# Kernel tuning notes

Measured on AMD Instinct MI355X. Metric: run time of the kernel, lower is better.

Reference implementation:

```python
import jax, jax.numpy as jnp
import numpy as np

N, E, F_IN, DIM, HEADS = 16384, 262144, 128, 64, 4
HID = DIM * HEADS  # 256
NEG = 0.2


def _lin(k, fan_in, fan_out):
    kw, kb = jax.random.split(k)
    s = 1.0 / np.sqrt(fan_in)
    return (jax.random.uniform(kw, (fan_in, fan_out), jnp.float32, -s, s),
            jax.random.uniform(kb, (fan_out,), jnp.float32, -s, s))


def setup_inputs() -> dict:
    key = jax.random.key(0)
    ks = jax.random.split(key, 20)
    x = jax.random.normal(ks[0], (N, F_IN), jnp.float32)
    edge_index = jax.random.randint(ks[1], (2, E), 0, N, jnp.int32)
    Win, b_in = _lin(ks[2], F_IN, DIM)
    Wskip, bskip = _lin(ks[3], DIM, HID)
    # conv1: in=DIM, out per head=DIM, heads=HEADS, concat -> HID
    Wl1, _ = _lin(ks[4], DIM, HID)
    Wr1, _ = _lin(ks[5], DIM, HID)
    att1 = jax.random.normal(ks[6], (HEADS, DIM), jnp.float32) * 0.1
    b1 = jnp.zeros((HID,), jnp.float32)
    # conv2: in=HID, out=HID, heads=1, concat=False
    Wl2, _ = _lin(ks[7], HID, HID)
    Wr2, _ = _lin(ks[8], HID, HID)
    att2 = jax.random.normal(ks[9], (1, HID), jnp.float32) * 0.1
    b2 = jnp.zeros((HID,), jnp.float32)
    # conv3: in=HID, out=HID, heads=1, concat=False
    Wl3, _ = _lin(ks[10], HID, HID)
    Wr3, _ = _lin(ks[11], HID, HID)
    att3 = jax.random.normal(ks[12], (1, HID), jnp.float32) * 0.1
    b3 = jnp.zeros((HID,), jnp.float32)
    Wm1, bm1 = _lin(ks[13], HID, DIM)
    Wm2, bm2 = _lin(ks[14], DIM, DIM)
    Wm3, bm3 = _lin(ks[15], DIM, 1)
    return dict(x=x, edge_index=edge_index, Win=Win, b_in=b_in,
                Wskip=Wskip, bskip=bskip,
                Wl1=Wl1, Wr1=Wr1, att1=att1, b1=b1,
                Wl2=Wl2, Wr2=Wr2, att2=att2, b2=b2,
                Wl3=Wl3, Wr3=Wr3, att3=att3, b3=b3,
                Wm1=Wm1, bm1=bm1, Wm2=Wm2, bm2=bm2, Wm3=Wm3, bm3=bm3)


def gatv2(x, src, dst, Wl, Wr, att, b, concat):
    # PyG GATv2Conv: x_l = lin_l(x)[src], x_r = lin_r(x)[dst]
    n = x.shape[0]
    H, D = att.shape
    xl = (x @ Wl).reshape(n, H, D)
    xr = (x @ Wr).reshape(n, H, D)
    e = jax.nn.leaky_relu(xl[src] + xr[dst], NEG)          # [E, H, D]
    logits = jnp.einsum('ehd,hd->eh', e, att)              # [E, H]
    m = jax.ops.segment_max(logits, dst, num_segments=n)   # per-dst softmax
    alpha = jnp.exp(logits - m[dst])
    denom = jax.ops.segment_sum(alpha, dst, num_segments=n)
    alpha = alpha / denom[dst]
    out = jax.ops.segment_sum(alpha[:, :, None] * xl[src], dst, num_segments=n)
    out = out.reshape(n, H * D) if concat else out.mean(axis=1)
    return out + b


def reference(x, edge_index, Win, b_in, Wskip, bskip,
              Wl1, Wr1, att1, b1, Wl2, Wr2, att2, b2,
              Wl3, Wr3, att3, b3, Wm1, bm1, Wm2, bm2, Wm3, bm3):
    n = x.shape[0]
    # add self loops (GATv2Conv default add_self_loops=True)
    loop = jnp.arange(n, dtype=edge_index.dtype)
    src = jnp.concatenate([edge_index[0], loop])
    dst = jnp.concatenate([edge_index[1], loop])

    h = jax.nn.relu(x @ Win + b_in)                         # [N, DIM]
    out1 = jax.nn.relu(gatv2(h, src, dst, Wl1, Wr1, att1, b1, True))
    out1 = out1 + (h @ Wskip + bskip)                       # [N, HID]
    out2 = jax.nn.relu(gatv2(out1, src, dst, Wl2, Wr2, att2, b2, False))
    out2 = out2 + out1
    out3 = jax.nn.relu(gatv2(out2, src, dst, Wl3, Wr3, att3, b3, False))
    out3 = out3 + out2
    out = jax.nn.relu(out3 @ Wm1 + bm1)
    out = jax.nn.relu(out @ Wm2 + bm2)
    out = out @ Wm3 + bm3                                   # [N, 1]
    return out.reshape(-1)
```

## Files before the change

kernel.cpp:

```cpp
#include <hip/hip_runtime.h>
#include <cstdint>
#include <cstddef>

#define N_NODES 16384
#define E_EDGES 262144
#define FIN     128
#define DIM     64
#define HID     256
#define NEG     0.2f

typedef _Float16 h8 __attribute__((ext_vector_type(8)));
typedef _Float16 h4 __attribute__((ext_vector_type(4)));
typedef _Float16 h2 __attribute__((ext_vector_type(2)));
typedef float    f32x4 __attribute__((ext_vector_type(4)));
typedef float    f32x2 __attribute__((ext_vector_type(2)));

__global__ __launch_bounds__(256) void hist_kernel(const int* __restrict__ dst,
                                                   int* __restrict__ cnt) {
    int i = blockIdx.x * 256 + threadIdx.x;
    if (i < E_EDGES) atomicAdd(&cnt[dst[i]], 1);
}

__global__ __launch_bounds__(256) void csr_scan_kernel(const int* __restrict__ cnt,
                                                       int* __restrict__ offs,
                                                       int* __restrict__ cursor) {
    __shared__ int wsum[4];
    int tid = threadIdx.x, lane = tid & 63, w = tid >> 6;
    int base = tid * 64;
    const int4* c4 = (const int4*)(cnt + base);
    int4 v[16];
    int s = 0;
#pragma unroll
    for (int i = 0; i < 16; ++i) {
        v[i] = c4[i];
        s += v[i].x + v[i].y + v[i].z + v[i].w;
    }
    int scan = s;
#pragma unroll
    for (int off = 1; off < 64; off <<= 1) {
        int t = __shfl_up(scan, off);
        if (lane >= off) scan += t;
    }
    if (lane == 63) wsum[w] = scan;
    __syncthreads();
    int wbase = 0;
#pragma unroll
    for (int i = 0; i < 4; ++i) if (i < w) wbase += wsum[i];
    int run = wbase + (scan - s);
#pragma unroll
    for (int i = 0; i < 16; ++i) {
        int4 o;
        o.x = run;
        o.y = o.x + v[i].x;
        o.z = o.y + v[i].y;
        o.w = o.z + v[i].z;
        *(int4*)(offs + base + 4 * i) = o;
        *(int4*)(cursor + base + 4 * i) = o;
        run = o.w + v[i].w;
    }
    if (tid == 255) offs[N_NODES] = run;
}

__global__ __launch_bounds__(256) void scatter_kernel(const int* __restrict__ src,
                                                      const int* __restrict__ dst,
                                                      int* __restrict__ cursor,
                                                      int* __restrict__ esrc) {
    int i = blockIdx.x * 256 + threadIdx.x;
    if (i < E_EDGES) {
        int p = atomicAdd(&cursor[dst[i]], 1);
        esrc[p] = src[i];
    }
}

struct PackJob { const float* W; _Float16* dst; int Ksrc, Nsrc, NT, colOff; };
struct PackJobs { PackJob j[10]; };

__global__ __launch_bounds__(256) void pack_all_kernel(PackJobs jobs, int* __restrict__ cnt) {
    int i = blockIdx.x * 256 + threadIdx.x;
    if (blockIdx.y == 10) {
        if (i < N_NODES) cnt[i] = 0;
        return;
    }
    PackJob jb = jobs.j[blockIdx.y];
    if (i < jb.Ksrc * jb.Nsrc) {
        int k = i / jb.Nsrc, n = i % jb.Nsrc;
        jb.dst[((size_t)(k >> 3) * jb.NT + jb.colOff + n) * 8 + (k & 7)] = (_Float16)jb.W[i];
    }
}

template<int K, bool RELU, bool O16, bool IN32>
__global__ __launch_bounds__(64) void mfma_n64_kernel(const void* __restrict__ Av,
                                                      const _Float16* __restrict__ Wp,
                                                      const float* __restrict__ bias,
                                                      void* __restrict__ outv) {
    int lane = threadIdx.x;
    int rowBase = blockIdx.x * 64;
    int l15 = lane & 15, l4 = lane >> 4;

    f32x4 acc[4][4] = {};
#pragma unroll
    for (int ks = 0; ks < K / 32; ++ks) {
        h8 af[4], bf[4];
#pragma unroll
        for (int mi = 0; mi < 4; ++mi) {
            if constexpr (IN32) {
                const float* ap = (const float*)Av + (size_t)(rowBase + mi * 16 + l15) * K + ks * 32 + l4 * 8;
                float4 a0 = *(const float4*)ap;
                float4 a1 = *(const float4*)(ap + 4);
                h8 v;
                v[0] = (_Float16)a0.x; v[1] = (_Float16)a0.y;
                v[2] = (_Float16)a0.z; v[3] = (_Float16)a0.w;
                v[4] = (_Float16)a1.x; v[5] = (_Float16)a1.y;
                v[6] = (_Float16)a1.z; v[7] = (_Float16)a1.w;
                af[mi] = v;
            } else {
                af[mi] = *(const h8*)((const _Float16*)Av + (size_t)(rowBase + mi * 16 + l15) * K + ks * 32 + l4 * 8);
            }
        }
#pragma unroll
        for (int ni = 0; ni < 4; ++ni)
            bf[ni] = *(const h8*)(Wp + ((size_t)(ks * 4 + l4) * 64 + ni * 16 + l15) * 8);
#pragma unroll
        for (int mi = 0; mi < 4; ++mi)
#pragma unroll
            for (int ni = 0; ni < 4; ++ni)
                acc[mi][ni] = __builtin_amdgcn_mfma_f32_16x16x32_f16(af[mi], bf[ni], acc[mi][ni], 0, 0, 0);
    }
#pragma unroll
    for (int mi = 0; mi < 4; ++mi)
#pragma unroll
        for (int ni = 0; ni < 4; ++ni) {
            int c = ni * 16 + l15;
            float bv = bias[c];
#pragma unroll
            for (int q = 0; q < 4; ++q) {
                int r = rowBase + mi * 16 + l4 * 4 + q;
                float v = acc[mi][ni][q] + bv;
                if (RELU) v = fmaxf(v, 0.f);
                if constexpr (O16) ((_Float16*)outv)[(size_t)r * 64 + c] = (_Float16)v;
                else               ((float*)outv)[(size_t)r * 64 + c] = v;
            }
        }
}

template<int K>
__global__ __launch_bounds__(256) void mfma_gemm_kernel(const _Float16* __restrict__ A,
                                                        const _Float16* __restrict__ Wp,
                                                        int NT,
                                                        _Float16* __restrict__ o16a,
                                                        _Float16* __restrict__ o16b,
                                                        float* __restrict__ o32,
                                                        const float* __restrict__ bias) {
    int tid = threadIdx.x;
    int lane = tid & 63, wid = tid >> 6;
    int wm = wid >> 1, wn = wid & 1;
    int rowBase = blockIdx.x * 128 + wm * 64;
    int colBase = blockIdx.y * 128 + wn * 64;
    int l15 = lane & 15, l4 = lane >> 4;

    f32x4 acc[4][4] = {};
#pragma unroll
    for (int ks = 0; ks < K / 32; ++ks) {
        h8 af[4], bf[4];
#pragma unroll
        for (int mi = 0; mi < 4; ++mi)
            af[mi] = *(const h8*)(A + (size_t)(rowBase + mi * 16 + l15) * K + ks * 32 + l4 * 8);
#pragma unroll
        for (int ni = 0; ni < 4; ++ni)
            bf[ni] = *(const h8*)(Wp + ((size_t)(ks * 4 + l4) * NT + colBase + ni * 16 + l15) * 8);
#pragma unroll
        for (int mi = 0; mi < 4; ++mi)
#pragma unroll
            for (int ni = 0; ni < 4; ++ni)
                acc[mi][ni] = __builtin_amdgcn_mfma_f32_16x16x32_f16(af[mi], bf[ni], acc[mi][ni], 0, 0, 0);
    }

    int seg = colBase >> 8;
    int cbase = colBase & 255;
    if (o32 != nullptr && seg == 2) {
#pragma unroll
        for (int mi = 0; mi < 4; ++mi)
#pragma unroll
            for (int ni = 0; ni < 4; ++ni) {
                int c = cbase + ni * 16 + l15;
                float bv = bias[c];
#pragma unroll
                for (int q = 0; q < 4; ++q) {
                    int r = rowBase + mi * 16 + l4 * 4 + q;
                    o32[(size_t)r * 256 + c] = acc[mi][ni][q] + bv;
                }
            }
    } else {
        _Float16* o = (seg == 0) ? o16a : o16b;
#pragma unroll
        for (int mi = 0; mi < 4; ++mi)
#pragma unroll
            for (int ni = 0; ni < 4; ++ni) {
                int c = cbase + ni * 16 + l15;
#pragma unroll
                for (int q = 0; q < 4; ++q) {
                    int r = rowBase + mi * 16 + l4 * 4 + q;
                    o[(size_t)r * 256 + c] = (_Float16)acc[mi][ni][q];
                }
            }
    }
}

template<int H, int OMODE>
__global__ __launch_bounds__(256) void gat_agg_kernel(const _Float16* __restrict__ xl,
                                                      const _Float16* __restrict__ xr,
                                                      const float* __restrict__ att,
                                                      const float* __restrict__ bias,
                                                      const float* __restrict__ resid,
                                                      const int* __restrict__ offs,
                                                      const int* __restrict__ esrc,
                                                      float* __restrict__ out,
                                                      _Float16* __restrict__ out16) {
    int tid = threadIdx.x;
    int wid = tid >> 6;
    int lane = tid & 63;
    int node = blockIdx.x * 4 + wid;
    int g  = lane >> 4;
    int li = lane & 15;

    h2 xrv[8];
    {
        const h8* xp = (const h8*)(xr + ((size_t)node << 8) + (li << 4));
        h8 a0 = xp[0], a1 = xp[1];
#pragma unroll
        for (int i = 0; i < 4; ++i) { xrv[i][0] = a0[2 * i]; xrv[i][1] = a0[2 * i + 1]; }
#pragma unroll
        for (int i = 0; i < 4; ++i) { xrv[4 + i][0] = a1[2 * i]; xrv[4 + i][1] = a1[2 * i + 1]; }
    }
    h2 attv[8];
    {
        const float4* ap = (const float4*)(att + (li << 4));
#pragma unroll
        for (int i = 0; i < 4; ++i) {
            float4 a = ap[i];
            attv[2 * i][0] = (_Float16)a.x; attv[2 * i][1] = (_Float16)a.y;
            attv[2 * i + 1][0] = (_Float16)a.z; attv[2 * i + 1][1] = (_Float16)a.w;
        }
    }
    const h2 negc = { (_Float16)NEG, (_Float16)NEG };

    int dbase = (li << 4) + (g << 2);
    float4 bv = *(const float4*)(bias + dbase);
    float4 rv = *(const float4*)(resid + ((size_t)node << 8) + dbase);

    float m = -1e30f, s = 0.f;
    f32x2 acc2[8];
#pragma unroll
    for (int i = 0; i < 8; ++i) acc2[i] = (f32x2){0.f, 0.f};

    int e0 = offs[node];
    int total = offs[node + 1] - e0 + 1;

    auto gather = [&](int srcn, h2* hv) {
        const h8* xp = (const h8*)(xl + ((size_t)srcn << 8) + (li << 4));
        h8 a0 = xp[0], a1 = xp[1];
#pragma unroll
        for (int i = 0; i < 4; ++i) { hv[i][0] = a0[2 * i]; hv[i][1] = a0[2 * i + 1]; }
#pragma unroll
        for (int i = 0; i < 4; ++i) { hv[4 + i][0] = a1[2 * i]; hv[4 + i][1] = a1[2 * i + 1]; }
    };
    auto logit = [&](const h2* hv) -> float {
        float p0 = 0.f, p1 = 0.f;
#pragma unroll
        for (int i = 0; i < 4; ++i) {
            h2 sum = hv[i] + xrv[i];
            h2 lr = __builtin_elementwise_max(sum, sum * negc);
            p0 = __builtin_amdgcn_fdot2(lr, attv[i], p0, false);
            h2 sum2 = hv[4 + i] + xrv[4 + i];
            h2 lr2 = __builtin_elementwise_max(sum2, sum2 * negc);
            p1 = __builtin_amdgcn_fdot2(lr2, attv[4 + i], p1, false);
        }
        float part = p0 + p1;
        part += __shfl_xor(part, 1);
        part += __shfl_xor(part, 2);
        if constexpr (H == 1) {
            part += __shfl_xor(part, 4);
            part += __shfl_xor(part, 8);
        }
        return part;
    };

    int vi = g;
    int sA = 0, sB = 0;
    if (vi + 4 < total) {
        sA = (vi == 0) ? node : esrc[e0 + vi - 1];
        sB = esrc[e0 + vi + 3];
    }
    for (; vi + 4 < total; vi += 8) {
        int nvi = vi + 8;
        int ia = e0 + nvi - 1; if (ia > E_EDGES - 1) ia = E_EDGES - 1;
        int ib = e0 + nvi + 3; if (ib > E_EDGES - 1) ib = E_EDGES - 1;
        int sA2 = esrc[ia];
        int sB2 = esrc[ib];

        h2 hA[8], hB[8];
        gather(sA, hA);
        gather(sB, hB);
        float lpA = logit(hA);
        float lpB = logit(hB);
        float mx = fmaxf(lpA, lpB);
        if (mx > m + 8.f) {
            float c  = __expf(m - mx);
            float pA = __expf(lpA - mx);
            float pB = __expf(lpB - mx);
            s = s * c + pA + pB;
#pragma unroll
            for (int i = 0; i < 8; ++i) {
                f32x2 t = acc2[i] * c;
                t[0] = fmaf(pA, (float)hA[i][0], t[0]);
                t[1] = fmaf(pA, (float)hA[i][1], t[1]);
                t[0] = fmaf(pB, (float)hB[i][0], t[0]);
                t[1] = fmaf(pB, (float)hB[i][1], t[1]);
                acc2[i] = t;
            }
            m = mx;
        } else {
            float pA = __expf(lpA - m);
            float pB = __expf(lpB - m);
            s += pA + pB;
#pragma unroll
            for (int i = 0; i < 8; ++i) {
                f32x2 t = acc2[i];
                t[0] = fmaf(pA, (float)hA[i][0], t[0]);
                t[1] = fmaf(pA, (float)hA[i][1], t[1]);
                t[0] = fmaf(pB, (float)hB[i][0], t[0]);
                t[1] = fmaf(pB, (float)hB[i][1], t[1]);
                acc2[i] = t;
            }
        }
        sA = sA2; sB = sB2;
    }
    for (; vi < total; vi += 4) {
        int srcn = (vi == 0) ? node : esrc[e0 + vi - 1];
        h2 hA[8];
        gather(srcn, hA);
        float lp = logit(hA);
        if (lp > m + 8.f) {
            float c = __expf(m - lp);
            float p = 1.f;
            s = s * c + p;
#pragma unroll
            for (int i = 0; i < 8; ++i) {
                f32x2 t = acc2[i] * c;
                t[0] = fmaf(p, (float)hA[i][0], t[0]);
                t[1] = fmaf(p, (float)hA[i][1], t[1]);
                acc2[i] = t;
            }
            m = lp;
        } else {
            float p = __expf(lp - m);
            s += p;
#pragma unroll
            for (int i = 0; i < 8; ++i) {
                f32x2 t = acc2[i];
                t[0] = fmaf(p, (float)hA[i][0], t[0]);
                t[1] = fmaf(p, (float)hA[i][1], t[1]);
                acc2[i] = t;
            }
        }
    }

#pragma unroll
    for (int mask = 16; mask <= 32; mask <<= 1) {
        float m2 = __shfl_xor(m, mask);
        float s2 = __shfl_xor(s, mask);
        float M = fmaxf(m, m2);
        float c1 = __expf(m - M);
        float c2 = __expf(m2 - M);
        s = s * c1 + s2 * c2;
#pragma unroll
        for (int i = 0; i < 8; ++i) {
            float ax = __shfl_xor(acc2[i][0], mask);
            float ay = __shfl_xor(acc2[i][1], mask);
            acc2[i][0] = acc2[i][0] * c1 + ax * c2;
            acc2[i][1] = acc2[i][1] * c1 + ay * c2;
        }
        m = M;
    }

    float inv = 1.f / s;
    float a0, a1v, a2, a3;
    if (g == 0)      { a0 = acc2[0][0]; a1v = acc2[0][1]; a2 = acc2[1][0]; a3 = acc2[1][1]; }
    else if (g == 1) { a0 = acc2[2][0]; a1v = acc2[2][1]; a2 = acc2[3][0]; a3 = acc2[3][1]; }
    else if (g == 2) { a0 = acc2[4][0]; a1v = acc2[4][1]; a2 = acc2[5][0]; a3 = acc2[5][1]; }
    else             { a0 = acc2[6][0]; a1v = acc2[6][1]; a2 = acc2[7][0]; a3 = acc2[7][1]; }
    float o0 = fmaxf(a0 * inv + bv.x, 0.f) + rv.x;
    float o1 = fmaxf(a1v * inv + bv.y, 0.f) + rv.y;
    float o2 = fmaxf(a2 * inv + bv.z, 0.f) + rv.z;
    float o3 = fmaxf(a3 * inv + bv.w, 0.f) + rv.w;
    if constexpr (OMODE != 2) {
        float4 ov = make_float4(o0, o1, o2, o3);
        *(float4*)(out + ((size_t)node << 8) + dbase) = ov;
    }
    if constexpr (OMODE != 0) {
        h4 hv;
        hv[0] = (_Float16)o0; hv[1] = (_Float16)o1;
        hv[2] = (_Float16)o2; hv[3] = (_Float16)o3;
        *(h4*)(out16 + ((size_t)node << 8) + dbase) = hv;
    }
}

__global__ __launch_bounds__(256) void mlp_head_kernel(const _Float16* __restrict__ A,
                                                       const _Float16* __restrict__ Wm1p,
                                                       const float* __restrict__ bm1,
                                                       const _Float16* __restrict__ Wm2p,
                                                       const float* __restrict__ bm2,
                                                       const float* __restrict__ Wm3,
                                                       const float* __restrict__ bm3,
                                                       float* __restrict__ out) {
    __shared__ _Float16 t1s[4][16][72];
    int tid = threadIdx.x;
    int lane = tid & 63, wid = tid >> 6;
    int rowBase = blockIdx.x * 64 + wid * 16;
    int l15 = lane & 15, l4 = lane >> 4;

    f32x4 acc[4] = {};
#pragma unroll
    for (int ks = 0; ks < 8; ++ks) {
        h8 af = *(const h8*)(A + (size_t)(rowBase + l15) * 256 + ks * 32 + l4 * 8);
        h8 bf[4];
#pragma unroll
        for (int ni = 0; ni < 4; ++ni)
            bf[ni] = *(const h8*)(Wm1p + ((size_t)(ks * 4 + l4) * 64 + ni * 16 + l15) * 8);
#pragma unroll
        for (int ni = 0; ni < 4; ++ni)
            acc[ni] = __builtin_amdgcn_mfma_f32_16x16x32_f16(af, bf[ni], acc[ni], 0, 0, 0);
    }
#pragma unroll
    for (int ni = 0; ni < 4; ++ni) {
        int c = ni * 16 + l15;
        float bv = bm1[c];
#pragma unroll
        for (int q = 0; q < 4; ++q)
            t1s[wid][l4 * 4 + q][c] = (_Float16)fmaxf(acc[ni][q] + bv, 0.f);
    }

    f32x4 acc2[4] = {};
#pragma unroll
    for (int ks = 0; ks < 2; ++ks) {
        h8 af = *(const h8*)&t1s[wid][l15][ks * 32 + l4 * 8];
        h8 bf[4];
#pragma unroll
        for (int ni = 0; ni < 4; ++ni)
            bf[ni] = *(const h8*)(Wm2p + ((size_t)(ks * 4 + l4) * 64 + ni * 16 + l15) * 8);
#pragma unroll
        for (int ni = 0; ni < 4; ++ni)
            acc2[ni] = __builtin_amdgcn_mfma_f32_16x16x32_f16(af, bf[ni], acc2[ni], 0, 0, 0);
    }

    float b3 = bm3[0];
    float b2v[4], w3v[4];
#pragma unroll
    for (int ni = 0; ni < 4; ++ni) {
        b2v[ni] = bm2[ni * 16 + l15];
        w3v[ni] = Wm3[ni * 16 + l15];
    }
#pragma unroll
    for (int q = 0; q < 4; ++q) {
        float part = 0.f;
#pragma unroll
        for (int ni = 0; ni < 4; ++ni)
            part += fmaxf(acc2[ni][q] + b2v[ni], 0.f) * w3v[ni];
        part += __shfl_xor(part, 1);
        part += __shfl_xor(part, 2);
        part += __shfl_xor(part, 4);
        part += __shfl_xor(part, 8);
        if (l15 == 0)
            out[rowBase + l4 * 4 + q] = part + b3;
    }
}

extern "C" void kernel_launch(void* const* d_in, const int* in_sizes, int n_in,
                              void* d_out, int out_size, void* d_ws, size_t ws_size,
                              hipStream_t stream) {
    const float* x     = (const float*)d_in[0];
    const int*   ei    = (const int*)d_in[1];
    const float* Win   = (const float*)d_in[2];
    const float* b_in  = (const float*)d_in[3];
    const float* Wskip = (const float*)d_in[4];
    const float* bskip = (const float*)d_in[5];
    const float* Wl1   = (const float*)d_in[6];
    const float* Wr1   = (const float*)d_in[7];
    const float* att1  = (const float*)d_in[8];
    const float* b1    = (const float*)d_in[9];
    const float* Wl2   = (const float*)d_in[10];
    const float* Wr2   = (const float*)d_in[11];
    const float* att2  = (const float*)d_in[12];
    const float* b2    = (const float*)d_in[13];
    const float* Wl3   = (const float*)d_in[14];
    const float* Wr3   = (const float*)d_in[15];
    const float* att3  = (const float*)d_in[16];
    const float* b3    = (const float*)d_in[17];
    const float* Wm1   = (const float*)d_in[18];
    const float* bm1   = (const float*)d_in[19];
    const float* Wm2   = (const float*)d_in[20];
    const float* bm2   = (const float*)d_in[21];
    const float* Wm3   = (const float*)d_in[22];
    const float* bm3   = (const float*)d_in[23];

    char* p = (char*)d_ws;
    auto alloc = [&](size_t bytes) { char* r = p; p += (bytes + 255) & ~(size_t)255; return r; };
    const size_t NN = N_NODES;
    float*    skip = (float*)alloc(NN * 256 * 4);
    float*    out1 = (float*)alloc(NN * 256 * 4);
    _Float16* o116 = (_Float16*)alloc(NN * 256 * 2);
    _Float16* o216 = (_Float16*)alloc(NN * 256 * 2);
    _Float16* o316 = o116;
    _Float16* h16  = (_Float16*)alloc(NN * 64 * 2);
    _Float16* xl16 = (_Float16*)alloc(NN * 256 * 2);
    _Float16* xr16 = (_Float16*)alloc(NN * 256 * 2);
    _Float16* Wp1  = (_Float16*)alloc((size_t)64 * 768 * 2);
    _Float16* Wp2  = (_Float16*)alloc((size_t)256 * 512 * 2);
    _Float16* Wp3  = (_Float16*)alloc((size_t)256 * 512 * 2);
    _Float16* Winp = (_Float16*)alloc((size_t)128 * 64 * 2);
    _Float16* Wm1p = (_Float16*)alloc((size_t)256 * 64 * 2);
    _Float16* Wm2p = (_Float16*)alloc((size_t)64 * 64 * 2);
    int* cnt    = (int*)alloc(N_NODES * 4);
    int* offs   = (int*)alloc((N_NODES + 1) * 4);
    int* cursor = (int*)alloc(N_NODES * 4);
    int* esrc   = (int*)alloc(E_EDGES * 4);

    const int* src = ei;
    const int* dst = ei + E_EDGES;

    PackJobs jobs = {{
        { Wl1,   Wp1,  64,  256, 768, 0   },
        { Wr1,   Wp1,  64,  256, 768, 256 },
        { Wskip, Wp1,  64,  256, 768, 512 },
        { Wl2,   Wp2,  256, 256, 512, 0   },
        { Wr2,   Wp2,  256, 256, 512, 256 },
        { Wl3,   Wp3,  256, 256, 512, 0   },
        { Wr3,   Wp3,  256, 256, 512, 256 },
        { Win,   Winp, 128, 64,  64,  0   },
        { Wm1,   Wm1p, 256, 64,  64,  0   },
        { Wm2,   Wm2p, 64,  64,  64,  0   },
    }};
    pack_all_kernel<<<dim3(256, 11), 256, 0, stream>>>(jobs, cnt);

    hist_kernel<<<E_EDGES / 256, 256, 0, stream>>>(dst, cnt);
    csr_scan_kernel<<<1, 256, 0, stream>>>(cnt, offs, cursor);
    scatter_kernel<<<E_EDGES / 256, 256, 0, stream>>>(src, dst, cursor, esrc);

    mfma_n64_kernel<128, true, true, true><<<N_NODES / 64, 64, 0, stream>>>(x, Winp, b_in, h16);

    mfma_gemm_kernel<64><<<dim3(128, 6), 256, 0, stream>>>(h16, Wp1, 768, xl16, xr16, skip, bskip);
    gat_agg_kernel<4, 1><<<N_NODES / 4, 256, 0, stream>>>(xl16, xr16, att1, b1, skip, offs, esrc, out1, o116);

    mfma_gemm_kernel<256><<<dim3(128, 4), 256, 0, stream>>>(o116, Wp2, 512, xl16, xr16, nullptr, nullptr);
    gat_agg_kernel<1, 1><<<N_NODES / 4, 256, 0, stream>>>(xl16, xr16, att2, b2, out1, offs, esrc, skip , o216);

    mfma_gemm_kernel<256><<<dim3(128, 4), 256, 0, stream>>>(o216, Wp3, 512, xl16, xr16, nullptr, nullptr);
    gat_agg_kernel<1, 2><<<N_NODES / 4, 256, 0, stream>>>(xl16, xr16, att3, b3, skip , offs, esrc, nullptr, o316);

    mlp_head_kernel<<<N_NODES / 64, 256, 0, stream>>>(o316, Wm1p, bm1, Wm2p, bm2, Wm3, bm3, (float*)d_out);
}
```

Before: 195.3 us.

## Merge CSR build stages with input projection and conv1 GEMM launches

Merges the edge histogram with the input projection GEMM into one launch, and the CSR prefix scan with the conv1 GEMM into another, by dispatching on block index. This drops two kernel launches and lets independent graph-preprocessing work run alongside dense matmuls. It also switches several streaming reads (xr, residual, MLP input) to nontemporal loads and simplifies an online-softmax update. The extra grid row and the block-index branching add some imbalance, and the scan now shares a launch with GEMM blocks.

```diff
diff --git a/kernel.cpp b/kernel.cpp
--- a/kernel.cpp
+++ b/kernel.cpp
@@ -15,17 +15,11 @@
 typedef float    f32x4 __attribute__((ext_vector_type(4)));
 typedef float    f32x2 __attribute__((ext_vector_type(2)));
 
-__global__ __launch_bounds__(256) void hist_kernel(const int* __restrict__ dst,
-                                                   int* __restrict__ cnt) {
-    int i = blockIdx.x * 256 + threadIdx.x;
-    if (i < E_EDGES) atomicAdd(&cnt[dst[i]], 1);
-}
-
-__global__ __launch_bounds__(256) void csr_scan_kernel(const int* __restrict__ cnt,
-                                                       int* __restrict__ offs,
-                                                       int* __restrict__ cursor) {
+__device__ __forceinline__ void csr_scan_body(const int* __restrict__ cnt,
+                                              int* __restrict__ offs,
+                                              int* __restrict__ cursor, int tid) {
     __shared__ int wsum[4];
-    int tid = threadIdx.x, lane = tid & 63, w = tid >> 6;
+    int lane = tid & 63, w = tid >> 6;
     int base = tid * 64;
     const int4* c4 = (const int4*)(cnt + base);
     int4 v[16];
@@ -61,42 +55,13 @@
     if (tid == 255) offs[N_NODES] = run;
 }
 
-__global__ __launch_bounds__(256) void scatter_kernel(const int* __restrict__ src,
-                                                      const int* __restrict__ dst,
-                                                      int* __restrict__ cursor,
-                                                      int* __restrict__ esrc) {
-    int i = blockIdx.x * 256 + threadIdx.x;
-    if (i < E_EDGES) {
-        int p = atomicAdd(&cursor[dst[i]], 1);
-        esrc[p] = src[i];
-    }
-}
-
-struct PackJob { const float* W; _Float16* dst; int Ksrc, Nsrc, NT, colOff; };
-struct PackJobs { PackJob j[10]; };
-
-__global__ __launch_bounds__(256) void pack_all_kernel(PackJobs jobs, int* __restrict__ cnt) {
-    int i = blockIdx.x * 256 + threadIdx.x;
-    if (blockIdx.y == 10) {
-        if (i < N_NODES) cnt[i] = 0;
-        return;
-    }
-    PackJob jb = jobs.j[blockIdx.y];
-    if (i < jb.Ksrc * jb.Nsrc) {
-        int k = i / jb.Nsrc, n = i % jb.Nsrc;
-        jb.dst[((size_t)(k >> 3) * jb.NT + jb.colOff + n) * 8 + (k & 7)] = (_Float16)jb.W[i];
-    }
-}
-
 template<int K, bool RELU, bool O16, bool IN32>
-__global__ __launch_bounds__(64) void mfma_n64_kernel(const void* __restrict__ Av,
-                                                      const _Float16* __restrict__ Wp,
-                                                      const float* __restrict__ bias,
-                                                      void* __restrict__ outv) {
-    int lane = threadIdx.x;
-    int rowBase = blockIdx.x * 64;
+__device__ __forceinline__ void mfma_n64_body(const void* __restrict__ Av,
+                                              const _Float16* __restrict__ Wp,
+                                              const float* __restrict__ bias,
+                                              void* __restrict__ outv,
+                                              int rowBase, int lane) {
     int l15 = lane & 15, l4 = lane >> 4;
-
     f32x4 acc[4][4] = {};
 #pragma unroll
     for (int ks = 0; ks < K / 32; ++ks) {
@@ -144,6 +109,130 @@
 }
 
 template<int K>
+__device__ __forceinline__ void mfma_gemm_body(const _Float16* __restrict__ A,
+                                               const _Float16* __restrict__ Wp,
+                                               int NT,
+                                               _Float16* __restrict__ o16a,
+                                               _Float16* __restrict__ o16b,
+                                               float* __restrict__ o32,
+                                               const float* __restrict__ bias,
+                                               int bx, int by, int tid) {
+    int lane = tid & 63, wid = tid >> 6;
+    int wm = wid >> 1, wn = wid & 1;
+    int rowBase = bx * 128 + wm * 64;
+    int colBase = by * 128 + wn * 64;
+    int l15 = lane & 15, l4 = lane >> 4;
+
+    f32x4 acc[4][4] = {};
+#pragma unroll
+    for (int ks = 0; ks < K / 32; ++ks) {
+        h8 af[4], bf[4];
+#pragma unroll
+        for (int mi = 0; mi < 4; ++mi)
+            af[mi] = *(const h8*)(A + (size_t)(rowBase + mi * 16 + l15) * K + ks * 32 + l4 * 8);
+#pragma unroll
+        for (int ni = 0; ni < 4; ++ni)
+            bf[ni] = *(const h8*)(Wp + ((size_t)(ks * 4 + l4) * NT + colBase + ni * 16 + l15) * 8);
+#pragma unroll
+        for (int mi = 0; mi < 4; ++mi)
+#pragma unroll
+            for (int ni = 0; ni < 4; ++ni)
+                acc[mi][ni] = __builtin_amdgcn_mfma_f32_16x16x32_f16(af[mi], bf[ni], acc[mi][ni], 0, 0, 0);
+    }
+
+    int seg = colBase >> 8;
+    int cbase = colBase & 255;
+    if (o32 != nullptr && seg == 2) {
+#pragma unroll
+        for (int mi = 0; mi < 4; ++mi)
+#pragma unroll
+            for (int ni = 0; ni < 4; ++ni) {
+                int c = cbase + ni * 16 + l15;
+                float bv = bias[c];
+#pragma unroll
+                for (int q = 0; q < 4; ++q) {
+                    int r = rowBase + mi * 16 + l4 * 4 + q;
+                    o32[(size_t)r * 256 + c] = acc[mi][ni][q] + bv;
+                }
+            }
+    } else {
+        _Float16* o = (seg == 0) ? o16a : o16b;
+#pragma unroll
+        for (int mi = 0; mi < 4; ++mi)
+#pragma unroll
+            for (int ni = 0; ni < 4; ++ni) {
+                int c = cbase + ni * 16 + l15;
+#pragma unroll
+                for (int q = 0; q < 4; ++q) {
+                    int r = rowBase + mi * 16 + l4 * 4 + q;
+                    o[(size_t)r * 256 + c] = (_Float16)acc[mi][ni][q];
+                }
+            }
+    }
+}
+
+struct PackJob { const float* W; _Float16* dst; int Ksrc, Nsrc, NT, colOff; };
+struct PackJobs { PackJob j[10]; };
+
+__global__ __launch_bounds__(256) void pack_all_kernel(PackJobs jobs, int* __restrict__ cnt) {
+    int i = blockIdx.x * 256 + threadIdx.x;
+    if (blockIdx.y == 10) {
+        if (i < N_NODES) cnt[i] = 0;
+        return;
+    }
+    PackJob jb = jobs.j[blockIdx.y];
+    if (i < jb.Ksrc * jb.Nsrc) {
+        int k = i / jb.Nsrc, n = i % jb.Nsrc;
+        jb.dst[((size_t)(k >> 3) * jb.NT + jb.colOff + n) * 8 + (k & 7)] = (_Float16)jb.W[i];
+    }
+}
+
+__global__ __launch_bounds__(256) void hist_inproj_kernel(const int* __restrict__ dst,
+                                                          int* __restrict__ cnt,
+                                                          const float* __restrict__ x,
+                                                          const _Float16* __restrict__ Winp,
+                                                          const float* __restrict__ b_in,
+                                                          _Float16* __restrict__ h16) {
+    int bx = blockIdx.x;
+    if (bx < E_EDGES / 256) {
+        int i = bx * 256 + threadIdx.x;
+        atomicAdd(&cnt[dst[i]], 1);
+        return;
+    }
+    int tid = threadIdx.x;
+    int wid = tid >> 6, lane = tid & 63;
+    int rowBase = (bx - E_EDGES / 256) * 256 + wid * 64;
+    mfma_n64_body<FIN, true, true, true>(x, Winp, b_in, h16, rowBase, lane);
+}
+
+__global__ __launch_bounds__(256) void conv1_scan_kernel(const _Float16* __restrict__ A,
+                                                         const _Float16* __restrict__ Wp,
+                                                         _Float16* __restrict__ xl16,
+                                                         _Float16* __restrict__ xr16,
+                                                         float* __restrict__ skip,
+                                                         const float* __restrict__ bskip,
+                                                         const int* __restrict__ cnt,
+                                                         int* __restrict__ offs,
+                                                         int* __restrict__ cursor) {
+    if (blockIdx.y == 6) {
+        if (blockIdx.x == 0) csr_scan_body(cnt, offs, cursor, threadIdx.x);
+        return;
+    }
+    mfma_gemm_body<64>(A, Wp, 768, xl16, xr16, skip, bskip, blockIdx.x, blockIdx.y, threadIdx.x);
+}
+
+__global__ __launch_bounds__(256) void scatter_kernel(const int* __restrict__ src,
+                                                      const int* __restrict__ dst,
+                                                      int* __restrict__ cursor,
+                                                      int* __restrict__ esrc) {
+    int i = blockIdx.x * 256 + threadIdx.x;
+    if (i < E_EDGES) {
+        int p = atomicAdd(&cursor[dst[i]], 1);
+        esrc[p] = src[i];
+    }
+}
+
+template<int K>
 __global__ __launch_bounds__(256) void mfma_gemm_kernel(const _Float16* __restrict__ A,
                                                         const _Float16* __restrict__ Wp,
                                                         int NT,
@@ -151,59 +240,7 @@
                                                         _Float16* __restrict__ o16b,
                                                         float* __restrict__ o32,
                                                         const float* __restrict__ bias) {
-    int tid = threadIdx.x;
-    int lane = tid & 63, wid = tid >> 6;
-    int wm = wid >> 1, wn = wid & 1;
-    int rowBase = blockIdx.x * 128 + wm * 64;
-    int colBase = blockIdx.y * 128 + wn * 64;
-    int l15 = lane & 15, l4 = lane >> 4;
-
-    f32x4 acc[4][4] = {};
-#pragma unroll
-    for (int ks = 0; ks < K / 32; ++ks) {
-        h8 af[4], bf[4];
-#pragma unroll
-        for (int mi = 0; mi < 4; ++mi)
-            af[mi] = *(const h8*)(A + (size_t)(rowBase + mi * 16 + l15) * K + ks * 32 + l4 * 8);
-#pragma unroll
-        for (int ni = 0; ni < 4; ++ni)
-            bf[ni] = *(const h8*)(Wp + ((size_t)(ks * 4 + l4) * NT + colBase + ni * 16 + l15) * 8);
-#pragma unroll
-        for (int mi = 0; mi < 4; ++mi)
-#pragma unroll
-            for (int ni = 0; ni < 4; ++ni)
-                acc[mi][ni] = __builtin_amdgcn_mfma_f32_16x16x32_f16(af[mi], bf[ni], acc[mi][ni], 0, 0, 0);
-    }
-
-    int seg = colBase >> 8;
-    int cbase = colBase & 255;
-    if (o32 != nullptr && seg == 2) {
-#pragma unroll
-        for (int mi = 0; mi < 4; ++mi)
-#pragma unroll
-            for (int ni = 0; ni < 4; ++ni) {
-                int c = cbase + ni * 16 + l15;
-                float bv = bias[c];
-#pragma unroll
-                for (int q = 0; q < 4; ++q) {
-                    int r = rowBase + mi * 16 + l4 * 4 + q;
-                    o32[(size_t)r * 256 + c] = acc[mi][ni][q] + bv;
-                }
-            }
-    } else {
-        _Float16* o = (seg == 0) ? o16a : o16b;
-#pragma unroll
-        for (int mi = 0; mi < 4; ++mi)
-#pragma unroll
-            for (int ni = 0; ni < 4; ++ni) {
-                int c = cbase + ni * 16 + l15;
-#pragma unroll
-                for (int q = 0; q < 4; ++q) {
-                    int r = rowBase + mi * 16 + l4 * 4 + q;
-                    o[(size_t)r * 256 + c] = (_Float16)acc[mi][ni][q];
-                }
-            }
-    }
+    mfma_gemm_body<K>(A, Wp, NT, o16a, o16b, o32, bias, blockIdx.x, blockIdx.y, threadIdx.x);
 }
 
 template<int H, int OMODE>
@@ -226,7 +263,8 @@
     h2 xrv[8];
     {
         const h8* xp = (const h8*)(xr + ((size_t)node << 8) + (li << 4));
-        h8 a0 = xp[0], a1 = xp[1];
+        h8 a0 = __builtin_nontemporal_load(xp);
+        h8 a1 = __builtin_nontemporal_load(xp + 1);
 #pragma unroll
         for (int i = 0; i < 4; ++i) { xrv[i][0] = a0[2 * i]; xrv[i][1] = a0[2 * i + 1]; }
 #pragma unroll
@@ -246,7 +284,7 @@
 
     int dbase = (li << 4) + (g << 2);
     float4 bv = *(const float4*)(bias + dbase);
-    float4 rv = *(const float4*)(resid + ((size_t)node << 8) + dbase);
+    f32x4 rv = __builtin_nontemporal_load((const f32x4*)(resid + ((size_t)node << 8) + dbase));
 
     float m = -1e30f, s = 0.f;
     f32x2 acc2[8];
@@ -342,13 +380,12 @@
         float lp = logit(hA);
         if (lp > m + 8.f) {
             float c = __expf(m - lp);
-            float p = 1.f;
-            s = s * c + p;
+            s = s * c + 1.f;
 #pragma unroll
             for (int i = 0; i < 8; ++i) {
                 f32x2 t = acc2[i] * c;
-                t[0] = fmaf(p, (float)hA[i][0], t[0]);
-                t[1] = fmaf(p, (float)hA[i][1], t[1]);
+                t[0] = t[0] + (float)hA[i][0];
+                t[1] = t[1] + (float)hA[i][1];
                 acc2[i] = t;
             }
             m = lp;
@@ -389,10 +426,10 @@
     else if (g == 1) { a0 = acc2[2][0]; a1v = acc2[2][1]; a2 = acc2[3][0]; a3 = acc2[3][1]; }
     else if (g == 2) { a0 = acc2[4][0]; a1v = acc2[4][1]; a2 = acc2[5][0]; a3 = acc2[5][1]; }
     else             { a0 = acc2[6][0]; a1v = acc2[6][1]; a2 = acc2[7][0]; a3 = acc2[7][1]; }
-    float o0 = fmaxf(a0 * inv + bv.x, 0.f) + rv.x;
-    float o1 = fmaxf(a1v * inv + bv.y, 0.f) + rv.y;
-    float o2 = fmaxf(a2 * inv + bv.z, 0.f) + rv.z;
-    float o3 = fmaxf(a3 * inv + bv.w, 0.f) + rv.w;
+    float o0 = fmaxf(a0 * inv + bv.x, 0.f) + rv[0];
+    float o1 = fmaxf(a1v * inv + bv.y, 0.f) + rv[1];
+    float o2 = fmaxf(a2 * inv + bv.z, 0.f) + rv[2];
+    float o3 = fmaxf(a3 * inv + bv.w, 0.f) + rv[3];
     if constexpr (OMODE != 2) {
         float4 ov = make_float4(o0, o1, o2, o3);
         *(float4*)(out + ((size_t)node << 8) + dbase) = ov;
@@ -422,7 +459,7 @@
     f32x4 acc[4] = {};
 #pragma unroll
     for (int ks = 0; ks < 8; ++ks) {
-        h8 af = *(const h8*)(A + (size_t)(rowBase + l15) * 256 + ks * 32 + l4 * 8);
+        h8 af = __builtin_nontemporal_load((const h8*)(A + (size_t)(rowBase + l15) * 256 + ks * 32 + l4 * 8));
         h8 bf[4];
 #pragma unroll
         for (int ni = 0; ni < 4; ++ni)
@@ -542,13 +579,14 @@
     }};
     pack_all_kernel<<<dim3(256, 11), 256, 0, stream>>>(jobs, cnt);
 
-    hist_kernel<<<E_EDGES / 256, 256, 0, stream>>>(dst, cnt);
-    csr_scan_kernel<<<1, 256, 0, stream>>>(cnt, offs, cursor);
+    hist_inproj_kernel<<<E_EDGES / 256 + N_NODES / 256, 256, 0, stream>>>(
+        dst, cnt, x, Winp, b_in, h16);
+
+    conv1_scan_kernel<<<dim3(128, 7), 256, 0, stream>>>(
+        h16, Wp1, xl16, xr16, skip, bskip, cnt, offs, cursor);
+
     scatter_kernel<<<E_EDGES / 256, 256, 0, stream>>>(src, dst, cursor, esrc);
 
-    mfma_n64_kernel<128, true, true, true><<<N_NODES / 64, 64, 0, stream>>>(x, Winp, b_in, h16);
-
-    mfma_gemm_kernel<64><<<dim3(128, 6), 256, 0, stream>>>(h16, Wp1, 768, xl16, xr16, skip, bskip);
     gat_agg_kernel<4, 1><<<N_NODES / 4, 256, 0, stream>>>(xl16, xr16, att1, b1, skip, offs, esrc, out1, o116);
 
     mfma_gemm_kernel<256><<<dim3(128, 4), 256, 0, stream>>>(o116, Wp2, 512, xl16, xr16, nullptr, nullptr);
```

New measurement: 194.8 us (median of 2 runs). Within noise of the previous version (-0.3%).
